# Kernel tuning notes

Measured on AMD Instinct MI355X. Metric: run time of the kernel, lower is better.

Reference implementation:

```python
import jax, jax.numpy as jnp
import numpy as np

HEAD_SIZE = 64
N_EMBD = 1024
BLOCK_SIZE = 2048


def setup_inputs() -> dict:
    key = jax.random.key(0)
    ks = jax.random.split(key, 7)
    B, T = 4, 2048
    s = 1.0 / np.sqrt(N_EMBD)
    return {
        "x": jax.random.normal(ks[0], (B, T, N_EMBD), dtype=jnp.float32),
        "Wq": jax.random.normal(ks[1], (N_EMBD, HEAD_SIZE), dtype=jnp.float32) * s,
        "bq": jnp.zeros((HEAD_SIZE,), dtype=jnp.float32),
        "Wk": jax.random.normal(ks[2], (N_EMBD, HEAD_SIZE), dtype=jnp.float32) * s,
        "bk": jnp.zeros((HEAD_SIZE,), dtype=jnp.float32),
        "Wv": jax.random.normal(ks[3], (N_EMBD, HEAD_SIZE), dtype=jnp.float32) * s,
        "bv": jnp.zeros((HEAD_SIZE,), dtype=jnp.float32),
    }


def reference(x, Wq, bq, Wk, bk, Wv, bv):
    # x: [B, T, n_embd]
    B, T, _ = x.shape
    q = x @ Wq + bq  # [B, T, H]
    k = x @ Wk + bk
    v = x @ Wv + bv
    # Faithful to source: divides by head_size**(-0.5) == multiplies by sqrt(head_size)
    scale = jnp.float32(HEAD_SIZE) ** 0.5
    scores = jnp.einsum("bqh,bkh->bqk", q, k) * scale  # [B, T, T]
    causal = jnp.tril(jnp.ones((T, T), dtype=bool))
    scores = jnp.where(causal, scores, -jnp.inf)
    attn = jax.nn.softmax(scores, axis=-1)  # dropout p=0.0 (eval)
    out = jnp.einsum("bqk,bkh->bqh", attn, v)  # [B, T, H]
    return out
```

## Files before the change

### kernel.cpp

```cpp
#include <hip/hip_runtime.h>
#include <math.h>

#define NE 1024
#define HS 64
#define TT 2048
#define QSC 11.541560327111707f

typedef __bf16    v8bf __attribute__((ext_vector_type(8)));
typedef _Float16  v8h  __attribute__((ext_vector_type(8)));
typedef float     v4f  __attribute__((ext_vector_type(4)));

#define MFMA_BF(a, b, c)  __builtin_amdgcn_mfma_f32_16x16x32_bf16((a), (b), (c), 0, 0, 0)
#define MFMA_F16(a, b, c) __builtin_amdgcn_mfma_f32_16x16x32_f16((a), (b), (c), 0, 0, 0)

__device__ __forceinline__ void gl_lds16(const void* g, void* l) {
    __builtin_amdgcn_global_load_lds(
        (const __attribute__((address_space(1))) unsigned int*)g,
        (__attribute__((address_space(3))) unsigned int*)l, 16, 0, 0);
}

__global__ __launch_bounds__(256) void prep_w(
    const float* __restrict__ Wq, const float* __restrict__ Wk,
    const float* __restrict__ Wv, char* __restrict__ imgW)
{
    __shared__ float t[64][65];
    const int bx = blockIdx.x, by = blockIdx.y;
    const float* W = (by == 0) ? Wq : ((by == 1) ? Wk : Wv);
    const int tid = threadIdx.x;
    const int cc = tid & 63, r4 = tid >> 6;
    #pragma unroll
    for (int p = 0; p < 16; ++p) {
        const int k = p * 4 + r4;
        t[k][cc] = W[(size_t)(bx * 64 + k) * HS + cc];
    }
    __syncthreads();
    #pragma unroll
    for (int e = 0; e < 4; ++e) {
        const int chunk = tid + e * 256;
        const int s2   = chunk >> 9;
        const int rem  = chunk & 511;
        const int ctl  = rem >> 7;
        const int rem2 = rem & 127;
        const int pl   = rem2 >> 6;
        const int rem3 = rem2 & 63;
        const int c    = rem3 >> 2;
        const int p16  = rem3 & 3;
        const int kb   = s2 * 32 + ((p16 ^ (c & 3)) << 3);
        const int ncol = ctl * 16 + c;
        v8bf o;
        #pragma unroll
        for (int j = 0; j < 8; ++j) {
            const float v = t[kb + j][ncol];
            const __bf16 h = (__bf16)v;
            o[j] = pl ? (__bf16)(v - (float)h) : h;
        }
        *(v8bf*)(imgW + (size_t)(bx * 2 + s2) * 24576
                 + (by * 4 + ctl) * 2048 + pl * 1024 + c * 64 + p16 * 16) = o;
    }
}

__global__ __launch_bounds__(256, 2) void proj(
    const float* __restrict__ x, const char* __restrict__ imgW,
    const float* __restrict__ bq, const float* __restrict__ bk,
    const float* __restrict__ bv,
    __bf16* __restrict__ qh, __bf16* __restrict__ ql,
    __bf16* __restrict__ kh, __bf16* __restrict__ kl,
    _Float16* __restrict__ vt)
{
    __shared__ __align__(16) char sbuf[2][26624];

    const int tid = threadIdx.x, lane = tid & 63, cg = tid >> 6;
    const int quad = lane >> 4, l16 = lane & 15;
    const int m0 = blockIdx.x * 16;

    const int xrow = tid >> 3;
    const int xc32 = ((tid & 7) >> 1) ^ (xrow & 3);
    const float* gx = x + (size_t)(m0 + xrow) * NE + xc32 * 8 + (tid & 1) * 4;
    const char*  gw = imgW + (size_t)tid * 16;

    v4f acc[3];
    #pragma unroll
    for (int i = 0; i < 3; ++i) acc[i] = (v4f){0.f, 0.f, 0.f, 0.f};

    #define STAGE(ks, b)  do {                                           \
        char* xb_ = sbuf[(b)];                                           \
        if (tid < 128) gl_lds16(gx + (ks) * 32, xb_ + tid * 16);         \
        const char* gws_ = gw + (size_t)(ks) * 24576;                    \
        _Pragma("unroll")                                                \
        for (int j_ = 0; j_ < 6; ++j_)                                   \
            gl_lds16(gws_ + j_ * 4096, xb_ + 2048 + tid * 16 + j_ * 4096); \
    } while (0)

    STAGE(0, 0);
    __syncthreads();

    for (int ks = 0; ks < 32; ++ks) {
        const int b = ks & 1;
        if (ks < 31) STAGE(ks + 1, b ^ 1);

        const char* xb = sbuf[b];
        const char* wb = xb + 2048;
        const int rl = l16;
        const int pA = quad ^ (rl & 3);
        const float4 a0 = *(const float4*)(xb + rl * 128 + pA * 32);
        const float4 a1 = *(const float4*)(xb + rl * 128 + pA * 32 + 16);
        const float av[8] = {a0.x, a0.y, a0.z, a0.w, a1.x, a1.y, a1.z, a1.w};
        v8bf ah, al;
        #pragma unroll
        for (int i = 0; i < 8; ++i) {
            const __bf16 h = (__bf16)av[i];
            ah[i] = h;
            al[i] = (__bf16)(av[i] - (float)h);
        }
        const int wo = l16 * 64 + ((quad ^ (l16 & 3)) << 4);
        #pragma unroll
        for (int j = 0; j < 3; ++j) {
            const char* base = wb + (cg * 3 + j) * 2048 + wo;
            const v8bf bh = *(const v8bf*)(base);
            const v8bf bl = *(const v8bf*)(base + 1024);
            acc[j] = MFMA_BF(ah, bh, acc[j]);
            acc[j] = MFMA_BF(ah, bl, acc[j]);
            acc[j] = MFMA_BF(al, bh, acc[j]);
        }
        __syncthreads();
    }
    #undef STAGE

    #pragma unroll
    for (int j = 0; j < 3; ++j) {
        const int n = cg * 48 + j * 16 + l16;
        const float bias = (n < 64) ? bq[n] : ((n < 128) ? bk[n - 64] : bv[n - 128]);
        #pragma unroll
        for (int reg = 0; reg < 4; ++reg) {
            const int row = m0 + quad * 4 + reg;
            const float v = acc[j][reg] + bias;
            if (n < 64) {
                const float s = v * QSC;
                const __bf16 hh = (__bf16)s;
                qh[(size_t)row * HS + n] = hh;
                ql[(size_t)row * HS + n] = (__bf16)(s - (float)hh);
            } else if (n < 128) {
                const __bf16 hh = (__bf16)v;
                kh[(size_t)row * HS + n - 64] = hh;
                kl[(size_t)row * HS + n - 64] = (__bf16)(v - (float)hh);
            } else {
                const int b2 = row >> 11, tt = row & 2047, hc = n - 128;
                vt[((size_t)(b2 * HS + hc)) * TT + tt] = (_Float16)v;
            }
        }
    }
}

__global__ __launch_bounds__(512, 2) void attn(
    const __bf16* __restrict__ qh, const __bf16* __restrict__ ql,
    const __bf16* __restrict__ kh, const __bf16* __restrict__ kl,
    const _Float16* __restrict__ vt, float* __restrict__ out)
{
    __shared__ __align__(16) char smem_raw[69632];
    _Float16* ps = (_Float16*)smem_raw;
    float*    os = (float*)smem_raw;
    __shared__ float sm[8][2][16], sl[8][2][16];

    const int tid = threadIdx.x, lane = tid & 63, w = tid >> 6;
    const int quad = lane >> 4, l16 = lane & 15;
    const int b = blockIdx.x & 3, pair = blockIdx.x >> 2;
    const int q0t[2] = {(127 - pair) * 16, pair * 16};
    const int ntk0 = (q0t[0] + 16 + 63) >> 6;
    const int ntk1 = (q0t[1] + 16 + 63) >> 6;
    const int total = ntk0 + ntk1;

    v8bf Qh0[2], Qh1[2], Ql0[2], Ql1[2];
    #pragma unroll
    for (int t = 0; t < 2; ++t) {
        const size_t qrow = ((size_t)b * TT + q0t[t] + l16) * HS;
        Qh0[t] = *(const v8bf*)(qh + qrow + quad * 8);
        Qh1[t] = *(const v8bf*)(qh + qrow + 32 + quad * 8);
        Ql0[t] = *(const v8bf*)(ql + qrow + quad * 8);
        Ql1[t] = *(const v8bf*)(ql + qrow + 32 + quad * 8);
    }

    const v8h vones = {(_Float16)1.f, (_Float16)1.f, (_Float16)1.f, (_Float16)1.f,
                       (_Float16)1.f, (_Float16)1.f, (_Float16)1.f, (_Float16)1.f};

    float mr0[4] = {-3e38f, -3e38f, -3e38f, -3e38f};
    float mr1[4] = {-3e38f, -3e38f, -3e38f, -3e38f};
    v4f o0[4], o1[4], l40, l41;
    #pragma unroll
    for (int i = 0; i < 4; ++i) {
        o0[i] = (v4f){0.f, 0.f, 0.f, 0.f};
        o1[i] = (v4f){0.f, 0.f, 0.f, 0.f};
    }
    l40 = (v4f){0.f, 0.f, 0.f, 0.f};
    l41 = (v4f){0.f, 0.f, 0.f, 0.f};

    _Float16* pw = ps + w * (16 * 72);

    auto doChunk = [&](int j0, int q0c, int t,
                       float (&mrow)[4], v4f (&o)[4], v4f &o4) {
        v8bf Kh[8], Kl[8];
        v8h  Vf[8];
        #pragma unroll
        for (int nt = 0; nt < 4; ++nt) {
            const size_t krow = ((size_t)b * TT + j0 + nt * 16 + l16) * HS;
            Kh[nt * 2]     = *(const v8bf*)(kh + krow + quad * 8);
            Kh[nt * 2 + 1] = *(const v8bf*)(kh + krow + 32 + quad * 8);
            Kl[nt * 2]     = *(const v8bf*)(kl + krow + quad * 8);
            Kl[nt * 2 + 1] = *(const v8bf*)(kl + krow + 32 + quad * 8);
        }
        #pragma unroll
        for (int nt = 0; nt < 4; ++nt) {
            const size_t vrow = ((size_t)(b * HS + nt * 16 + l16)) * TT + j0;
            Vf[nt * 2]     = *(const v8h*)(vt + vrow + quad * 8);
            Vf[nt * 2 + 1] = *(const v8h*)(vt + vrow + 32 + quad * 8);
        }
        v4f s[4];
        #pragma unroll
        for (int i = 0; i < 4; ++i) s[i] = (v4f){0.f, 0.f, 0.f, 0.f};
        #pragma unroll
        for (int nt = 0; nt < 4; ++nt) {
            s[nt] = MFMA_BF(Qh0[t], Kh[nt * 2],     s[nt]);
            s[nt] = MFMA_BF(Qh1[t], Kh[nt * 2 + 1], s[nt]);
            s[nt] = MFMA_BF(Qh0[t], Kl[nt * 2],     s[nt]);
            s[nt] = MFMA_BF(Qh1[t], Kl[nt * 2 + 1], s[nt]);
            s[nt] = MFMA_BF(Ql0[t], Kh[nt * 2],     s[nt]);
            s[nt] = MFMA_BF(Ql1[t], Kh[nt * 2 + 1], s[nt]);
        }
        const int irow = q0c + quad * 4;
        float mx[4] = {-3e38f, -3e38f, -3e38f, -3e38f};
        #pragma unroll
        for (int nt = 0; nt < 4; ++nt)
            #pragma unroll
            for (int reg = 0; reg < 4; ++reg) {
                if (j0 + nt * 16 + l16 > irow + reg) s[nt][reg] = -3e38f;
                mx[reg] = fmaxf(mx[reg], s[nt][reg]);
            }
        #pragma unroll
        for (int off = 8; off; off >>= 1)
            #pragma unroll
            for (int reg = 0; reg < 4; ++reg)
                mx[reg] = fmaxf(mx[reg], __shfl_xor(mx[reg], off));
        float al[4];
        #pragma unroll
        for (int reg = 0; reg < 4; ++reg) {
            const float mn = fmaxf(mrow[reg], mx[reg]);
            al[reg] = exp2f(mrow[reg] - mn);
            mrow[reg] = mn;
        }
        #pragma unroll
        for (int nt = 0; nt < 4; ++nt)
            #pragma unroll
            for (int reg = 0; reg < 4; ++reg) {
                const float p = (j0 + nt * 16 + l16 > irow + reg)
                                    ? 0.f : exp2f(s[nt][reg] - mrow[reg]);
                pw[(quad * 4 + reg) * 72 + nt * 16 + l16] = (_Float16)p;
            }
        #pragma unroll
        for (int nt = 0; nt < 4; ++nt)
            #pragma unroll
            for (int reg = 0; reg < 4; ++reg)
                o[nt][reg] *= al[reg];
        #pragma unroll
        for (int reg = 0; reg < 4; ++reg)
            o4[reg] *= al[reg];
        const v8h Pa0 = *(const v8h*)(pw + l16 * 72 + quad * 8);
        const v8h Pa1 = *(const v8h*)(pw + l16 * 72 + 32 + quad * 8);
        #pragma unroll
        for (int nt = 0; nt < 4; ++nt) {
            o[nt] = MFMA_F16(Pa0, Vf[nt * 2],     o[nt]);
            o[nt] = MFMA_F16(Pa1, Vf[nt * 2 + 1], o[nt]);
        }
        o4 = MFMA_F16(Pa0, vones, o4);
        o4 = MFMA_F16(Pa1, vones, o4);
    };

    for (int c = w; c < total; c += 8) {
        if (c < ntk0) doChunk(c * 64,          q0t[0], 0, mr0, o0, l40);
        else          doChunk((c - ntk0) * 64, q0t[1], 1, mr1, o1, l41);
    }

    if (l16 == 0) {
        #pragma unroll
        for (int reg = 0; reg < 4; ++reg) {
            sm[w][0][quad * 4 + reg] = mr0[reg];
            sl[w][0][quad * 4 + reg] = l40[reg];
            sm[w][1][quad * 4 + reg] = mr1[reg];
            sl[w][1][quad * 4 + reg] = l41[reg];
        }
    }
    __syncthreads();

    #pragma unroll
    for (int t = 0; t < 2; ++t) {
        float sc[4];
        #pragma unroll
        for (int reg = 0; reg < 4; ++reg) {
            const int r = quad * 4 + reg;
            float M = sm[0][t][r];
            #pragma unroll
            for (int i = 1; i < 8; ++i) M = fmaxf(M, sm[i][t][r]);
            const float mw = t ? mr1[reg] : mr0[reg];
            sc[reg] = exp2f(mw - M);
        }
        float* ow = os + (size_t)(w * 2 + t) * (16 * 68);
        #pragma unroll
        for (int nt = 0; nt < 4; ++nt)
            #pragma unroll
            for (int reg = 0; reg < 4; ++reg) {
                const v4f& oo = t ? o1[nt] : o0[nt];
                ow[(quad * 4 + reg) * 68 + nt * 16 + l16] = oo[reg] * sc[reg];
            }
    }
    __syncthreads();

    #pragma unroll
    for (int kk = 0; kk < 4; ++kk) {
        const int g = w * 4 + kk;
        const int t = g >> 4, m = g & 15;
        float M = sm[0][t][m];
        #pragma unroll
        for (int i = 1; i < 8; ++i) M = fmaxf(M, sm[i][t][m]);
        float L = 0.f, val = 0.f;
        #pragma unroll
        for (int i = 0; i < 8; ++i) {
            L   += sl[i][t][m] * exp2f(sm[i][t][m] - M);
            val += os[(size_t)(i * 2 + t) * (16 * 68) + m * 68 + lane];
        }
        out[((size_t)b * TT + q0t[t] + m) * HS + lane] = val / L;
    }
}

extern "C" void kernel_launch(void* const* d_in, const int* in_sizes, int n_in,
                              void* d_out, int out_size, void* d_ws, size_t ws_size,
                              hipStream_t stream)
{
    const float* x  = (const float*)d_in[0];
    const float* Wq = (const float*)d_in[1];
    const float* bq = (const float*)d_in[2];
    const float* Wk = (const float*)d_in[3];
    const float* bk = (const float*)d_in[4];
    const float* Wv = (const float*)d_in[5];
    const float* bv = (const float*)d_in[6];
    float* out = (float*)d_out;

    const int rows = in_sizes[0] / NE;
    char* p = (char*)d_ws;
    char* imgW = p;                           p += (size_t)32 * 24576;
    __bf16* qhb = (__bf16*)p;                 p += (size_t)rows * HS * 2;
    __bf16* qlb = (__bf16*)p;                 p += (size_t)rows * HS * 2;
    __bf16* khb = (__bf16*)p;                 p += (size_t)rows * HS * 2;
    __bf16* klb = (__bf16*)p;                 p += (size_t)rows * HS * 2;
    _Float16* vtb = (_Float16*)p;             p += (size_t)rows * HS * 2;

    prep_w<<<dim3(16, 3), 256, 0, stream>>>(Wq, Wk, Wv, imgW);
    proj<<<rows / 16, 256, 0, stream>>>(x, imgW, bq, bk, bv,
                                        qhb, qlb, khb, klb, vtb);
    attn<<<rows / 32, 512, 0, stream>>>(qhb, qlb, khb, klb, vtb, out);
}
```

Baseline: 138.7 us.

## Load projection operands directly into registers with prefetch instead of LDS staging

The projection kernel no longer stages x and weight tiles through double-buffered shared memory with global-to-LDS loads and per-step barriers. Each wave now loads its own x fragments and transposed bf16 hi/lo weight fragments straight from global memory into registers, prefetching several k-steps ahead in a register ring. Blocks double to 512 threads covering 32 rows, and prep_w writes a plain transposed layout. This removes LDS traffic and barriers, but each wave now fetches weights from global memory on its own, which relies on cache hits, and register pressure goes up.

Result: slower. 168.1 us (+21.2%).

```diff
diff --git a/kernel.cpp b/kernel.cpp
--- a/kernel.cpp
+++ b/kernel.cpp
@@ -13,98 +13,74 @@
 #define MFMA_BF(a, b, c)  __builtin_amdgcn_mfma_f32_16x16x32_bf16((a), (b), (c), 0, 0, 0)
 #define MFMA_F16(a, b, c) __builtin_amdgcn_mfma_f32_16x16x32_f16((a), (b), (c), 0, 0, 0)
 
-__device__ __forceinline__ void gl_lds16(const void* g, void* l) {
-    __builtin_amdgcn_global_load_lds(
-        (const __attribute__((address_space(1))) unsigned int*)g,
-        (__attribute__((address_space(3))) unsigned int*)l, 16, 0, 0);
-}
-
 __global__ __launch_bounds__(256) void prep_w(
     const float* __restrict__ Wq, const float* __restrict__ Wk,
-    const float* __restrict__ Wv, char* __restrict__ imgW)
+    const float* __restrict__ Wv, __bf16* __restrict__ wth, __bf16* __restrict__ wtl)
 {
     __shared__ float t[64][65];
-    const int bx = blockIdx.x, by = blockIdx.y;
-    const float* W = (by == 0) ? Wq : ((by == 1) ? Wk : Wv);
+    const int k0 = blockIdx.x * 64, n0 = blockIdx.y * 64;
+    const float* W = (n0 == 0) ? Wq : ((n0 == 64) ? Wk : Wv);
     const int tid = threadIdx.x;
-    const int cc = tid & 63, r4 = tid >> 6;
+    const int c = tid & 63, r4 = tid >> 6;
     #pragma unroll
     for (int p = 0; p < 16; ++p) {
         const int k = p * 4 + r4;
-        t[k][cc] = W[(size_t)(bx * 64 + k) * HS + cc];
+        t[k][c] = W[(size_t)(k0 + k) * HS + c];
     }
     __syncthreads();
     #pragma unroll
-    for (int e = 0; e < 4; ++e) {
-        const int chunk = tid + e * 256;
-        const int s2   = chunk >> 9;
-        const int rem  = chunk & 511;
-        const int ctl  = rem >> 7;
-        const int rem2 = rem & 127;
-        const int pl   = rem2 >> 6;
-        const int rem3 = rem2 & 63;
-        const int c    = rem3 >> 2;
-        const int p16  = rem3 & 3;
-        const int kb   = s2 * 32 + ((p16 ^ (c & 3)) << 3);
-        const int ncol = ctl * 16 + c;
-        v8bf o;
-        #pragma unroll
-        for (int j = 0; j < 8; ++j) {
-            const float v = t[kb + j][ncol];
-            const __bf16 h = (__bf16)v;
-            o[j] = pl ? (__bf16)(v - (float)h) : h;
-        }
-        *(v8bf*)(imgW + (size_t)(bx * 2 + s2) * 24576
-                 + (by * 4 + ctl) * 2048 + pl * 1024 + c * 64 + p16 * 16) = o;
+    for (int p = 0; p < 16; ++p) {
+        const int n = p * 4 + r4;
+        const float w = t[c][n];
+        const __bf16 h = (__bf16)w;
+        const size_t o = (size_t)(n0 + n) * NE + k0 + c;
+        wth[o] = h;
+        wtl[o] = (__bf16)(w - (float)h);
     }
 }
 
-__global__ __launch_bounds__(256, 2) void proj(
-    const float* __restrict__ x, const char* __restrict__ imgW,
+__global__ __launch_bounds__(512, 2) void proj(
+    const float* __restrict__ x,
+    const __bf16* __restrict__ wth, const __bf16* __restrict__ wtl,
     const float* __restrict__ bq, const float* __restrict__ bk,
     const float* __restrict__ bv,
     __bf16* __restrict__ qh, __bf16* __restrict__ ql,
     __bf16* __restrict__ kh, __bf16* __restrict__ kl,
     _Float16* __restrict__ vt)
 {
-    __shared__ __align__(16) char sbuf[2][26624];
-
-    const int tid = threadIdx.x, lane = tid & 63, cg = tid >> 6;
+    const int tid = threadIdx.x, lane = tid & 63, w = tid >> 6;
+    const int cg = w & 3, mt = w >> 2;
     const int quad = lane >> 4, l16 = lane & 15;
-    const int m0 = blockIdx.x * 16;
-
-    const int xrow = tid >> 3;
-    const int xc32 = ((tid & 7) >> 1) ^ (xrow & 3);
-    const float* gx = x + (size_t)(m0 + xrow) * NE + xc32 * 8 + (tid & 1) * 4;
-    const char*  gw = imgW + (size_t)tid * 16;
+    const int m0 = blockIdx.x * 32;
+
+    const float*  xp  = x + (size_t)(m0 + mt * 16 + l16) * NE + quad * 8;
+    const __bf16* bhp = wth + (size_t)(cg * 48 + l16) * NE + quad * 8;
+    const __bf16* blp = wtl + (size_t)(cg * 48 + l16) * NE + quad * 8;
 
     v4f acc[3];
     #pragma unroll
     for (int i = 0; i < 3; ++i) acc[i] = (v4f){0.f, 0.f, 0.f, 0.f};
 
-    #define STAGE(ks, b)  do {                                           \
-        char* xb_ = sbuf[(b)];                                           \
-        if (tid < 128) gl_lds16(gx + (ks) * 32, xb_ + tid * 16);         \
-        const char* gws_ = gw + (size_t)(ks) * 24576;                    \
-        _Pragma("unroll")                                                \
-        for (int j_ = 0; j_ < 6; ++j_)                                   \
-            gl_lds16(gws_ + j_ * 4096, xb_ + 2048 + tid * 16 + j_ * 4096); \
-    } while (0)
-
-    STAGE(0, 0);
-    __syncthreads();
-
+    float4 xa[4][2];
+    v8bf wbh[2][3], wbl[2][3];
+    #pragma unroll
+    for (int d = 0; d < 4; ++d) {
+        xa[d][0] = *(const float4*)(xp + d * 32);
+        xa[d][1] = *(const float4*)(xp + d * 32 + 4);
+    }
+    #pragma unroll
+    for (int d = 0; d < 2; ++d)
+        #pragma unroll
+        for (int j = 0; j < 3; ++j) {
+            wbh[d][j] = *(const v8bf*)(bhp + (size_t)j * 16 * NE + d * 32);
+            wbl[d][j] = *(const v8bf*)(blp + (size_t)j * 16 * NE + d * 32);
+        }
+
+    #pragma unroll
     for (int ks = 0; ks < 32; ++ks) {
-        const int b = ks & 1;
-        if (ks < 31) STAGE(ks + 1, b ^ 1);
-
-        const char* xb = sbuf[b];
-        const char* wb = xb + 2048;
-        const int rl = l16;
-        const int pA = quad ^ (rl & 3);
-        const float4 a0 = *(const float4*)(xb + rl * 128 + pA * 32);
-        const float4 a1 = *(const float4*)(xb + rl * 128 + pA * 32 + 16);
-        const float av[8] = {a0.x, a0.y, a0.z, a0.w, a1.x, a1.y, a1.z, a1.w};
+        const int cx = ks & 3, cw = ks & 1;
+        const float4 c0 = xa[cx][0], c1 = xa[cx][1];
+        const float av[8] = {c0.x, c0.y, c0.z, c0.w, c1.x, c1.y, c1.z, c1.w};
         v8bf ah, al;
         #pragma unroll
         for (int i = 0; i < 8; ++i) {
@@ -112,19 +88,27 @@
             ah[i] = h;
             al[i] = (__bf16)(av[i] - (float)h);
         }
-        const int wo = l16 * 64 + ((quad ^ (l16 & 3)) << 4);
-        #pragma unroll
-        for (int j = 0; j < 3; ++j) {
-            const char* base = wb + (cg * 3 + j) * 2048 + wo;
-            const v8bf bh = *(const v8bf*)(base);
-            const v8bf bl = *(const v8bf*)(base + 1024);
-            acc[j] = MFMA_BF(ah, bh, acc[j]);
-            acc[j] = MFMA_BF(ah, bl, acc[j]);
-            acc[j] = MFMA_BF(al, bh, acc[j]);
-        }
-        __syncthreads();
-    }
-    #undef STAGE
+        acc[0] = MFMA_BF(ah, wbh[cw][0], acc[0]);
+        acc[1] = MFMA_BF(ah, wbh[cw][1], acc[1]);
+        acc[2] = MFMA_BF(ah, wbh[cw][2], acc[2]);
+        acc[0] = MFMA_BF(ah, wbl[cw][0], acc[0]);
+        acc[1] = MFMA_BF(ah, wbl[cw][1], acc[1]);
+        acc[2] = MFMA_BF(ah, wbl[cw][2], acc[2]);
+        acc[0] = MFMA_BF(al, wbh[cw][0], acc[0]);
+        acc[1] = MFMA_BF(al, wbh[cw][1], acc[1]);
+        acc[2] = MFMA_BF(al, wbh[cw][2], acc[2]);
+        if (ks + 4 < 32) {
+            xa[cx][0] = *(const float4*)(xp + (ks + 4) * 32);
+            xa[cx][1] = *(const float4*)(xp + (ks + 4) * 32 + 4);
+        }
+        if (ks + 2 < 32) {
+            #pragma unroll
+            for (int j = 0; j < 3; ++j) {
+                wbh[cw][j] = *(const v8bf*)(bhp + (size_t)j * 16 * NE + (ks + 2) * 32);
+                wbl[cw][j] = *(const v8bf*)(blp + (size_t)j * 16 * NE + (ks + 2) * 32);
+            }
+        }
+    }
 
     #pragma unroll
     for (int j = 0; j < 3; ++j) {
@@ -132,7 +116,7 @@
         const float bias = (n < 64) ? bq[n] : ((n < 128) ? bk[n - 64] : bv[n - 128]);
         #pragma unroll
         for (int reg = 0; reg < 4; ++reg) {
-            const int row = m0 + quad * 4 + reg;
+            const int row = m0 + mt * 16 + quad * 4 + reg;
             const float v = acc[j][reg] + bias;
             if (n < 64) {
                 const float s = v * QSC;
@@ -344,15 +328,16 @@
 
     const int rows = in_sizes[0] / NE;
     char* p = (char*)d_ws;
-    char* imgW = p;                           p += (size_t)32 * 24576;
+    __bf16* wth = (__bf16*)p;                 p += (size_t)192 * NE * 2;
+    __bf16* wtl = (__bf16*)p;                 p += (size_t)192 * NE * 2;
     __bf16* qhb = (__bf16*)p;                 p += (size_t)rows * HS * 2;
     __bf16* qlb = (__bf16*)p;                 p += (size_t)rows * HS * 2;
     __bf16* khb = (__bf16*)p;                 p += (size_t)rows * HS * 2;
     __bf16* klb = (__bf16*)p;                 p += (size_t)rows * HS * 2;
     _Float16* vtb = (_Float16*)p;             p += (size_t)rows * HS * 2;
 
-    prep_w<<<dim3(16, 3), 256, 0, stream>>>(Wq, Wk, Wv, imgW);
-    proj<<<rows / 16, 256, 0, stream>>>(x, imgW, bq, bk, bv,
+    prep_w<<<dim3(16, 3), 256, 0, stream>>>(Wq, Wk, Wv, wth, wtl);
+    proj<<<rows / 32, 512, 0, stream>>>(x, wth, wtl, bq, bk, bv,
                                         qhb, qlb, khb, klb, vtb);
     attn<<<rows / 32, 512, 0, stream>>>(qhb, qlb, khb, klb, vtb, out);
 }
```

## Triple-buffer projection loads with vmcnt-based waits and per-wave x staging

Applied to the files above, without the earlier changes.

Moves the projection kernel from double to triple buffering in LDS, issuing loads two K-steps ahead. It replaces the full __syncthreads with an explicit s_waitcnt on vmcnt plus a barrier, so the step being computed only waits for its own loads while the next step's loads stay in flight. The x tile is now staged by every wave with 4-byte direct-to-LDS loads instead of half the threads issuing 16-byte loads. The costs are about 26 KB more LDS per block, which may limit two-blocks-per-CU occupancy, more load instructions for x, and a hand-coded waitcnt immediate that must match the per-stage load count.

Result: no change. 136.4 us (-1.6%).

```diff
diff --git a/kernel.cpp b/kernel.cpp
--- a/kernel.cpp
+++ b/kernel.cpp
@@ -18,6 +18,20 @@
         (const __attribute__((address_space(1))) unsigned int*)g,
         (__attribute__((address_space(3))) unsigned int*)l, 16, 0, 0);
 }
+__device__ __forceinline__ void gl_lds4(const void* g, void* l) {
+    __builtin_amdgcn_global_load_lds(
+        (const __attribute__((address_space(1))) unsigned int*)g,
+        (__attribute__((address_space(3))) unsigned int*)l, 4, 0, 0);
+}
+
+#define SYNC_VM(imm) do {                                   \
+    __asm__ __volatile__("" ::: "memory");                  \
+    __builtin_amdgcn_s_waitcnt(imm);                        \
+    __builtin_amdgcn_s_barrier();                           \
+    __asm__ __volatile__("" ::: "memory");                  \
+} while (0)
+#define WAIT_VM8  0x0F78
+#define WAIT_VM0  0x0F70
 
 __global__ __launch_bounds__(256) void prep_w(
     const float* __restrict__ Wq, const float* __restrict__ Wk,
@@ -67,38 +81,38 @@
     __bf16* __restrict__ kh, __bf16* __restrict__ kl,
     _Float16* __restrict__ vt)
 {
-    __shared__ __align__(16) char sbuf[2][26624];
+    __shared__ __align__(16) char sbuf[3][26624];
 
     const int tid = threadIdx.x, lane = tid & 63, cg = tid >> 6;
     const int quad = lane >> 4, l16 = lane & 15;
     const int m0 = blockIdx.x * 16;
 
-    const int xrow = tid >> 3;
-    const int xc32 = ((tid & 7) >> 1) ^ (xrow & 3);
-    const float* gx = x + (size_t)(m0 + xrow) * NE + xc32 * 8 + (tid & 1) * 4;
-    const char*  gw = imgW + (size_t)tid * 16;
+    const int wv = cg;
+    const int xr0 = wv * 4 + (lane >> 5);
+    const int xr1 = xr0 + 2;
+    const int xp  = (lane >> 3) & 3;
+    const int xj  = lane & 7;
+    const float* gx0 = x + (size_t)(m0 + xr0) * NE + ((xp ^ (xr0 & 3)) << 3) + xj;
+    const float* gx1 = x + (size_t)(m0 + xr1) * NE + ((xp ^ (xr1 & 3)) << 3) + xj;
+    const int xl0 = wv * 512 + (lane & 63) * 4;
+    const int xl1 = xl0 + 256;
+    const char* gw = imgW + (size_t)tid * 16;
 
     v4f acc[3];
     #pragma unroll
     for (int i = 0; i < 3; ++i) acc[i] = (v4f){0.f, 0.f, 0.f, 0.f};
 
-    #define STAGE(ks, b)  do {                                           \
-        char* xb_ = sbuf[(b)];                                           \
-        if (tid < 128) gl_lds16(gx + (ks) * 32, xb_ + tid * 16);         \
-        const char* gws_ = gw + (size_t)(ks) * 24576;                    \
-        _Pragma("unroll")                                                \
-        for (int j_ = 0; j_ < 6; ++j_)                                   \
-            gl_lds16(gws_ + j_ * 4096, xb_ + 2048 + tid * 16 + j_ * 4096); \
+    #define STAGE(ks, xb_)  do {                                          \
+        gl_lds4(gx0 + (ks) * 32, (xb_) + xl0);                            \
+        gl_lds4(gx1 + (ks) * 32, (xb_) + xl1);                            \
+        const char* gws_ = gw + (size_t)(ks) * 24576;                     \
+        _Pragma("unroll")                                                 \
+        for (int j_ = 0; j_ < 6; ++j_)                                    \
+            gl_lds16(gws_ + j_ * 4096, (xb_) + 2048 + tid * 16 + j_ * 4096); \
     } while (0)
 
-    STAGE(0, 0);
-    __syncthreads();
-
-    for (int ks = 0; ks < 32; ++ks) {
-        const int b = ks & 1;
-        if (ks < 31) STAGE(ks + 1, b ^ 1);
-
-        const char* xb = sbuf[b];
+    auto compute = [&](int ks) {
+        const char* xb = sbuf[ks % 3];
         const char* wb = xb + 2048;
         const int rl = l16;
         const int pA = quad ^ (rl & 3);
@@ -122,8 +136,17 @@
             acc[j] = MFMA_BF(ah, bl, acc[j]);
             acc[j] = MFMA_BF(al, bh, acc[j]);
         }
-        __syncthreads();
-    }
+    };
+
+    STAGE(0, sbuf[0]);
+    STAGE(1, sbuf[1]);
+    for (int ks = 0; ks < 31; ++ks) {
+        SYNC_VM(WAIT_VM8);
+        if (ks + 2 < 32) STAGE(ks + 2, sbuf[(ks + 2) % 3]);
+        compute(ks);
+    }
+    SYNC_VM(WAIT_VM0);
+    compute(31);
     #undef STAGE
 
     #pragma unroll
```
